# Kernel optimization log

Hardware: AMD Instinct MI355X
Metric: run time of the kernel (lower is better)

Reference implementation:

```python
import jax, jax.numpy as jnp
import numpy as np

D, B, L, LS, DH, DU, QK, CD = 5, 2048, 50, 50, 128, 128, 64, 64
EPS = 1e-5

def _l2norm(x):
    n = jnp.linalg.norm(x, axis=-1, keepdims=True)
    return x / jnp.maximum(n, 1e-12)

def setup_inputs() -> dict:
    key = jax.random.key(0)
    ks = jax.random.split(key, 20)
    def pw(k, shape):
        return jax.random.normal(k, shape, dtype=jnp.float32) * 0.02
    return {
        "u": jax.random.normal(ks[0], (B, DU), jnp.float32),
        "H_intra": jax.random.normal(ks[1], (D, B, L, DH), jnp.float32),
        "H_share": jax.random.normal(ks[2], (B, LS, DH), jnp.float32),
        "h": jax.random.normal(ks[3], (B, DH), jnp.float32),
        "domain_ids": jax.random.randint(ks[4], (B,), 0, D),
        "Wq": pw(ks[5], (DU + DH, QK)), "bq": jnp.zeros((QK,), jnp.float32),
        "Wki": pw(ks[6], (DH, QK)), "bki": jnp.zeros((QK,), jnp.float32),
        "Wvi": pw(ks[7], (DH, QK)), "bvi": jnp.zeros((QK,), jnp.float32),
        "Wks": pw(ks[8], (DH, QK)), "bks": jnp.zeros((QK,), jnp.float32),
        "Wvs": pw(ks[9], (DH, QK)), "bvs": jnp.zeros((QK,), jnp.float32),
        "Wf": pw(ks[10], (2 * QK, CD)), "bf": jnp.zeros((CD,), jnp.float32),
        "Wgb": pw(ks[11], (CD, 2 * DH)), "bgb": jnp.zeros((2 * DH,), jnp.float32),
    }

def reference(u, H_intra, H_share, h, domain_ids, Wq, bq, Wki, bki, Wvi, bvi,
              Wks, bks, Wvs, bvs, Wf, bf, Wgb, bgb):
    scale = jnp.sqrt(jnp.asarray(QK, jnp.float32))
    # ---- CDIExtractor (domain loop batched over leading D axis) ----
    c = H_intra.mean(axis=2)                                   # [D,B,DH] ctx = mean over L
    u_b = jnp.broadcast_to(u, (D, B, DU))
    Q = jnp.concatenate([u_b, c], axis=-1) @ Wq + bq            # [D,B,QK]
    Ki = H_intra @ Wki + bki                                    # [D,B,L,QK]
    Vi = H_intra @ Wvi + bvi
    Ks = H_share @ Wks + bks                                    # [B,LS,QK]
    Vs = H_share @ Wvs + bvs
    a_i = jax.nn.softmax(jnp.einsum('dbq,dblq->dbl', Q, Ki) / scale, axis=-1)
    h_i = jnp.einsum('dbl,dblq->dbq', a_i, Vi)                  # [D,B,QK]
    a_s = jax.nn.softmax(jnp.einsum('dbq,blq->dbl', Q, Ks) / scale, axis=-1)
    h_s = jnp.einsum('dbl,blq->dbq', a_s, Vs)                   # [D,B,QK]
    z = jnp.concatenate([h_i, h_s], axis=-1) @ Wf + bf          # [D,B,CD]
    # ---- contrastive loss (stacked as [B,D,QK] like torch.stack(dim=1)) ----
    hi = jnp.transpose(h_i, (1, 0, 2))
    hs = jnp.transpose(h_s, (1, 0, 2))
    ni, ns = _l2norm(hi), _l2norm(hs)
    pos_sim = jnp.sum(ni * ns, axis=-1)                         # [B,D]
    all_sim = jnp.einsum('bdq,beq->bde', ni, ni)                # [B,D,D]
    denom = jnp.exp(all_sim).sum(axis=-1)                       # [B,D]
    L_con = -jnp.mean(jnp.log(jnp.exp(pos_sim) / (denom + 1e-8) + 1e-8))
    # ---- CDIRInjector_Norm (domain-masked AdaNorm, segment statistics) ----
    onehot = jax.nn.one_hot(domain_ids, D, dtype=h.dtype)       # [B,D]
    cnt = jnp.maximum(onehot.sum(axis=0), 1.0)                  # [D]
    mean_d = (onehot.T @ h) / cnt[:, None]                      # [D,DH]
    var_d = (onehot.T @ (h * h)) / cnt[:, None] - mean_d ** 2   # biased var
    mu = mean_d[domain_ids]                                     # [B,DH]
    va = var_d[domain_ids]
    h_norm = (h - mu) / jnp.sqrt(va + EPS)
    z_sel = z[domain_ids, jnp.arange(B)]                        # [B,CD]
    gb = z_sel @ Wgb + bgb
    gamma, beta = jnp.split(gb, 2, axis=-1)
    out = gamma * h_norm + beta + h                             # [B,DH]
    return out, L_con
```

## Files before the change

### kernel.cpp

```cpp
#include <hip/hip_runtime.h>
#include <math.h>

#define D 5
#define B 2048
#define L 50
#define LS 50
#define DH 128
#define DU 128
#define QK 64
#define CD 64
#define EPS 1e-5f

__device__ __forceinline__ float wsum(float v) {
    v += __shfl_xor(v, 1, 64);
    v += __shfl_xor(v, 2, 64);
    v += __shfl_xor(v, 4, 64);
    v += __shfl_xor(v, 8, 64);
    v += __shfl_xor(v, 16, 64);
    v += __shfl_xor(v, 32, 64);
    return v;
}

__device__ __forceinline__ float wmax(float v) {
    v = fmaxf(v, __shfl_xor(v, 1, 64));
    v = fmaxf(v, __shfl_xor(v, 2, 64));
    v = fmaxf(v, __shfl_xor(v, 4, 64));
    v = fmaxf(v, __shfl_xor(v, 8, 64));
    v = fmaxf(v, __shfl_xor(v, 16, 64));
    v = fmaxf(v, __shfl_xor(v, 32, 64));
    return v;
}

__device__ __forceinline__ float gsum32(float v) {
    v += __shfl_xor(v, 1, 64);
    v += __shfl_xor(v, 2, 64);
    v += __shfl_xor(v, 4, 64);
    v += __shfl_xor(v, 8, 64);
    v += __shfl_xor(v, 16, 64);
    return v;
}

__device__ __forceinline__ float dot4(float4 a, float4 b) {
    return a.x * b.x + a.y * b.y + a.z * b.z + a.w * b.w;
}

__global__ __launch_bounds__(256) void ksetup(
    const float* __restrict__ u,
    const float* __restrict__ Wq, const float* __restrict__ bq,
    const float* __restrict__ Wki, const float* __restrict__ Wks,
    float* __restrict__ Gi, float* __restrict__ Gs,
    float* __restrict__ qu_i, float* __restrict__ qu_s)
{
    const int t = threadIdx.x;
    if (blockIdx.x < DH) {
        __shared__ float sWqc[QK];
        const int j = blockIdx.x;
        if (t < QK) sWqc[t] = Wq[(DU + j) * QK + t];
        __syncthreads();
        const int k = t & 127;
        const float* Wk = (t < 128) ? Wki : Wks;
        const float4* Wr = (const float4*)(Wk + k * QK);
        const float4* cq = (const float4*)sWqc;
        float acc = 0.f;
        #pragma unroll
        for (int q4 = 0; q4 < 16; ++q4) acc += dot4(Wr[q4], cq[q4]);
        if (t < 128) Gi[j * DH + k] = acc;
        else Gs[j * DH + k] = acc;
    } else {
        __shared__ float sPart[4 * QK];
        __shared__ float sQu[QK];
        const int b = blockIdx.x - DH;
        const int lane = t & 63, wave = t >> 6;
        float acc = 0.f;
        const int k0 = wave * 32;
        #pragma unroll 8
        for (int i = 0; i < 32; ++i) {
            int k = k0 + i;
            acc += u[(size_t)b * DU + k] * Wq[k * QK + lane];
        }
        sPart[wave * QK + lane] = acc;
        __syncthreads();
        if (t < QK) sQu[t] = bq[t] + sPart[t] + sPart[64 + t] + sPart[128 + t] + sPart[192 + t];
        __syncthreads();
        const int k = t & 127;
        const float* Wk = (t < 128) ? Wki : Wks;
        const float4* Wr = (const float4*)(Wk + k * QK);
        const float4* cq = (const float4*)sQu;
        float acc2 = 0.f;
        #pragma unroll
        for (int q4 = 0; q4 < 16; ++q4) acc2 += dot4(Wr[q4], cq[q4]);
        if (t < 128) qu_i[(size_t)b * DH + k] = acc2;
        else qu_s[(size_t)b * DH + k] = acc2;
    }
}

__global__ __launch_bounds__(256, 4) void kin(
    const float* __restrict__ Hi,
    const float* __restrict__ Gi, const float* __restrict__ Gs,
    const float* __restrict__ qu_i, const float* __restrict__ qu_s,
    const float* __restrict__ Wvi, const float* __restrict__ bvi,
    float* __restrict__ qvs_w,
    float* __restrict__ hi_w)
{
    __shared__ float4 sP4[256];
    __shared__ float sC2[2 * DH];
    __shared__ float sQVi[2 * DH];
    __shared__ float sSc[128];
    __shared__ float sA[128];
    __shared__ float sVagg[2 * DH];
    __shared__ float sPA[256], sPB[256];

    const int b0 = blockIdx.x * 2;
    const int d = blockIdx.y;
    const int t = threadIdx.x;
    const int lane = t & 63, wave = t >> 6;
    const int bb = t >> 7;
    const int tb = t & 127;
    const int gg = tb >> 5;
    const int col4 = t & 31;
    const int nr = (gg < 2) ? 13 : 12;
    const float* sPf = (const float*)sP4;

    const float* Hbase = Hi + ((size_t)d * B + (b0 + bb)) * (L * DH);
    float4 h4[13];
    #pragma unroll
    for (int k = 0; k < 13; ++k)
        if (k < nr) h4[k] = *(const float4*)(Hbase + (gg + 4 * k) * DH + 4 * col4);

    {
        float4 cs = make_float4(0.f, 0.f, 0.f, 0.f);
        #pragma unroll
        for (int k = 0; k < 13; ++k)
            if (k < nr) { cs.x += h4[k].x; cs.y += h4[k].y; cs.z += h4[k].z; cs.w += h4[k].w; }
        sP4[t] = cs;
    }
    __syncthreads();
    {
        const int bbc = t >> 7, col = t & 127;
        float s = sPf[bbc * 512 + col] + sPf[bbc * 512 + 128 + col]
                + sPf[bbc * 512 + 256 + col] + sPf[bbc * 512 + 384 + col];
        sC2[col * 2 + bbc] = s * (1.0f / (float)L);
    }
    __syncthreads();

    {
        const int mat = t >> 7, k = t & 127;
        const float* G = mat ? Gs : Gi;
        const float* qum = mat ? qu_s : qu_i;
        float a0 = qum[(size_t)b0 * DH + k];
        float a1 = qum[(size_t)(b0 + 1) * DH + k];
        const float2* c2 = (const float2*)sC2;
        #pragma unroll 8
        for (int j = 0; j < DH; ++j) {
            float g = G[j * DH + k];
            float2 c = c2[j];
            a0 += c.x * g;
            a1 += c.y * g;
        }
        if (mat == 0) { sQVi[k] = a0; sQVi[DH + k] = a1; }
        else {
            qvs_w[((size_t)d * B + b0) * DH + k] = a0;
            qvs_w[((size_t)d * B + b0 + 1) * DH + k] = a1;
        }
    }
    __syncthreads();

    {
        float4 qv = ((const float4*)sQVi)[bb * 32 + col4];
        #pragma unroll
        for (int k = 0; k < 13; ++k)
            if (k < nr) {
                float p = dot4(h4[k], qv);
                p = gsum32(p);
                if (col4 == 0) sSc[bb * 64 + gg + 4 * k] = p * 0.125f;
            }
    }
    __syncthreads();
    if (wave < 2) {
        float s = (lane < L) ? sSc[wave * 64 + lane] : -3.0e38f;
        float m = wmax(s);
        float e = (lane < L) ? expf(s - m) : 0.f;
        float ssum = wsum(e);
        if (lane < L) sA[wave * 64 + lane] = e / ssum;
    }
    __syncthreads();

    {
        float4 va = make_float4(0.f, 0.f, 0.f, 0.f);
        #pragma unroll
        for (int k = 0; k < 13; ++k)
            if (k < nr) {
                float a = sA[bb * 64 + gg + 4 * k];
                va.x += a * h4[k].x; va.y += a * h4[k].y;
                va.z += a * h4[k].z; va.w += a * h4[k].w;
            }
        sP4[t] = va;
    }
    __syncthreads();
    {
        const int bbc = t >> 7, col = t & 127;
        sVagg[bbc * 128 + col] = sPf[bbc * 512 + col] + sPf[bbc * 512 + 128 + col]
                               + sPf[bbc * 512 + 256 + col] + sPf[bbc * 512 + 384 + col];
    }
    __syncthreads();

    {
        const int q = t & 63, kq = t >> 6;
        const int k0 = kq * 32;
        float a0 = 0.f, a1 = 0.f;
        #pragma unroll 8
        for (int i = 0; i < 32; ++i) {
            int k = k0 + i;
            float w = Wvi[k * QK + q];
            a0 += sVagg[k] * w;
            a1 += sVagg[128 + k] * w;
        }
        sPA[kq * 64 + q] = a0;
        sPB[kq * 64 + q] = a1;
    }
    __syncthreads();
    if (t < 128) {
        const int bw = t >> 6, q = t & 63;
        const float* P = bw ? sPB : sPA;
        hi_w[((size_t)d * B + b0 + bw) * QK + q] =
            bvi[q] + P[q] + P[64 + q] + P[128 + q] + P[192 + q];
    }
}

__global__ __launch_bounds__(256) void kstat(
    const float* __restrict__ h, const int* __restrict__ dom_ids,
    float* __restrict__ gsum, float* __restrict__ gsq, float* __restrict__ gcnt)
{
    __shared__ float sS[D * DH], sQ2[D * DH], sCnt[D];
    const int t = threadIdx.x;
    const int b0 = blockIdx.x * 32;
    for (int i = t; i < D * DH; i += 256) { sS[i] = 0.f; sQ2[i] = 0.f; }
    if (t < D) sCnt[t] = 0.f;
    __syncthreads();
    const int col = t & 127, half = t >> 7;
    for (int rr = 0; rr < 16; ++rr) {
        int b = b0 + rr * 2 + half;
        float v = h[(size_t)b * DH + col];
        int dm = dom_ids[b];
        atomicAdd(&sS[dm * DH + col], v);
        atomicAdd(&sQ2[dm * DH + col], v * v);
        if (col == 0) atomicAdd(&sCnt[dm], 1.f);
    }
    __syncthreads();
    for (int i = t; i < D * DH; i += 256) {
        atomicAdd(&gsum[i], sS[i]);
        atomicAdd(&gsq[i], sQ2[i]);
    }
    if (t < D) atomicAdd(&gcnt[t], sCnt[t]);
}

__global__ __launch_bounds__(256, 4) void ksh(
    const float* __restrict__ Hs,
    const float* __restrict__ qvs_w,
    const float* __restrict__ Wvs, const float* __restrict__ bvs,
    float* __restrict__ hs_w)
{
    __shared__ float4 sQV4[160];
    __shared__ float sS[D * 64];
    __shared__ float4 sVP4[1280];
    __shared__ float sVA[D * DH];

    const int b = blockIdx.x;
    const int t = threadIdx.x;
    const int lane = t & 63;
    const int wave = t >> 6;
    const int g = t >> 5;
    const int col4 = t & 31;
    const int nrow = (g < 2) ? 7 : 6;
    float* sBigF = (float*)sVP4;

    const float* Hbase = Hs + (size_t)b * LS * DH;
    float4 h4[7];
    #pragma unroll
    for (int k = 0; k < 7; ++k)
        if (k < nrow) h4[k] = *(const float4*)(Hbase + (g + 8 * k) * DH + 4 * col4);
    if (t < 160) {
        int dd = t >> 5, c4 = t & 31;
        sQV4[t] = *(const float4*)(qvs_w + ((size_t)dd * B + b) * DH + 4 * c4);
    }
    __syncthreads();

    #pragma unroll
    for (int dd = 0; dd < D; ++dd) {
        float4 qv = sQV4[dd * 32 + col4];
        #pragma unroll
        for (int k = 0; k < 7; ++k)
            if (k < nrow) {
                float p = dot4(h4[k], qv);
                p = gsum32(p);
                if (col4 == 0) sS[dd * 64 + g + 8 * k] = p * 0.125f;
            }
    }
    __syncthreads();
    for (int dd = wave; dd < D; dd += 4) {
        float s = (lane < LS) ? sS[dd * 64 + lane] : -3.0e38f;
        float m = wmax(s);
        float e = (lane < LS) ? expf(s - m) : 0.f;
        float ssum = wsum(e);
        if (lane < LS) sS[dd * 64 + lane] = e / ssum;
    }
    __syncthreads();

    {
        float4 va[D];
        #pragma unroll
        for (int dd = 0; dd < D; ++dd) va[dd] = make_float4(0.f, 0.f, 0.f, 0.f);
        #pragma unroll
        for (int k = 0; k < 7; ++k)
            if (k < nrow) {
                float4 hv = h4[k];
                #pragma unroll
                for (int dd = 0; dd < D; ++dd) {
                    float a = sS[dd * 64 + g + 8 * k];
                    va[dd].x += a * hv.x; va[dd].y += a * hv.y;
                    va[dd].z += a * hv.z; va[dd].w += a * hv.w;
                }
            }
        #pragma unroll
        for (int dd = 0; dd < D; ++dd) sVP4[dd * 256 + t] = va[dd];
    }
    __syncthreads();
    for (int o = t; o < D * DH; o += 256) {
        int dd = o >> 7, col = o & 127;
        float s = 0.f;
        #pragma unroll
        for (int gg = 0; gg < 8; ++gg) s += sBigF[dd * 1024 + gg * 128 + col];
        sVA[o] = s;
    }
    __syncthreads();

    #pragma unroll
    for (int j = 0; j < 5; ++j) {
        int tau = t + j * 256;
        int kq = tau / 320;
        int o = tau - kq * 320;
        int dd = o >> 6, q = o & 63;
        float acc = 0.f;
        const int k0 = kq * 32;
        #pragma unroll 8
        for (int i = 0; i < 32; ++i) {
            int k = k0 + i;
            acc += sVA[dd * 128 + k] * Wvs[k * QK + q];
        }
        sBigF[tau] = acc;
    }
    __syncthreads();
    for (int o = t; o < D * QK; o += 256) {
        int dd = o >> 6, q = o & 63;
        hs_w[((size_t)dd * B + b) * QK + q] =
            bvs[q] + sBigF[o] + sBigF[o + 320] + sBigF[o + 640] + sBigF[o + 960];
    }
}

__global__ __launch_bounds__(256) void kfin(
    const float* __restrict__ h, const int* __restrict__ dom_ids,
    const float* __restrict__ hi_w, const float* __restrict__ hs_w,
    const float* __restrict__ Wf, const float* __restrict__ bf,
    const float* __restrict__ Wgb, const float* __restrict__ bgb,
    const float* __restrict__ gsum, const float* __restrict__ gsq,
    const float* __restrict__ gcnt,
    float* __restrict__ out, float* __restrict__ loss_out)
{
    __shared__ float sHI[D * QK], sHS[D * QK];
    __shared__ float sInv[16], sSim[32], sZ[QK], sPartZ[256], sGB[256];

    const int b = blockIdx.x;
    const int t = threadIdx.x;
    const int lane = t & 63;
    const int wave = t >> 6;
    const int dm = dom_ids[b];

    if (t < 80) {
        int dd = t >> 4, q4 = t & 15;
        ((float4*)sHI)[t] = *(const float4*)(hi_w + ((size_t)dd * B + b) * QK + 4 * q4);
        ((float4*)sHS)[t] = *(const float4*)(hs_w + ((size_t)dd * B + b) * QK + 4 * q4);
    }
    __syncthreads();

    for (int v = wave; v < 2 * D; v += 4) {
        float x = (v < D) ? sHI[v * QK + lane] : sHS[(v - D) * QK + lane];
        float ss = wsum(x * x);
        if (lane == 0) sInv[v] = 1.0f / fmaxf(sqrtf(ss), 1e-12f);
    }
    __syncthreads();
    for (int p = wave; p < 30; p += 4) {
        float s;
        if (p < 25) {
            int dd = p / 5, e = p - dd * 5;
            s = wsum(sHI[dd * QK + lane] * sHI[e * QK + lane] * sInv[dd] * sInv[e]);
        } else {
            int dd = p - 25;
            s = wsum(sHI[dd * QK + lane] * sHS[dd * QK + lane] * sInv[dd] * sInv[D + dd]);
        }
        if (lane == 0) sSim[p] = s;
    }
    __syncthreads();
    if (t == 0) {
        float tot = 0.f;
        #pragma unroll
        for (int dd = 0; dd < D; ++dd) {
            float den = 0.f;
            #pragma unroll
            for (int e = 0; e < D; ++e) den += expf(sSim[dd * 5 + e]);
            tot += logf(expf(sSim[25 + dd]) / (den + 1e-8f) + 1e-8f);
        }
        atomicAdd(loss_out, -tot / (float)(B * D));
    }

    {
        const int kq = wave, q = lane;
        float acc = 0.f;
        const int k0 = kq * 32;
        #pragma unroll 8
        for (int i = 0; i < 32; ++i) {
            int k = k0 + i;
            float x = (k < QK) ? sHI[dm * QK + k] : sHS[dm * QK + (k - QK)];
            acc += x * Wf[k * CD + q];
        }
        sPartZ[t] = acc;
    }
    __syncthreads();
    if (t < QK) sZ[t] = bf[t] + sPartZ[t] + sPartZ[64 + t] + sPartZ[128 + t] + sPartZ[192 + t];
    __syncthreads();

    {
        float acc = bgb[t];
        #pragma unroll 8
        for (int k = 0; k < CD; ++k) acc += sZ[k] * Wgb[k * (2 * DH) + t];
        sGB[t] = acc;
    }
    __syncthreads();

    if (t < DH) {
        float c = fmaxf(gcnt[dm], 1.0f);
        float mu = gsum[dm * DH + t] / c;
        float va = gsq[dm * DH + t] / c - mu * mu;
        float hv = h[(size_t)b * DH + t];
        float hn = (hv - mu) / sqrtf(va + EPS);
        out[(size_t)b * DH + t] = sGB[t] * hn + sGB[DH + t] + hv;
    }
}

extern "C" void kernel_launch(void* const* d_in, const int* in_sizes, int n_in,
                              void* d_out, int out_size, void* d_ws, size_t ws_size,
                              hipStream_t stream)
{
    (void)in_sizes; (void)n_in; (void)out_size; (void)ws_size;
    const float* u   = (const float*)d_in[0];
    const float* Hi  = (const float*)d_in[1];
    const float* Hs  = (const float*)d_in[2];
    const float* h   = (const float*)d_in[3];
    const int*   dom = (const int*)d_in[4];
    const float* Wq  = (const float*)d_in[5];
    const float* bq  = (const float*)d_in[6];
    const float* Wki = (const float*)d_in[7];
    const float* Wvi = (const float*)d_in[9];
    const float* bvi = (const float*)d_in[10];
    const float* Wks = (const float*)d_in[11];
    const float* Wvs = (const float*)d_in[13];
    const float* bvs = (const float*)d_in[14];
    const float* Wf  = (const float*)d_in[15];
    const float* bf  = (const float*)d_in[16];
    const float* Wgb = (const float*)d_in[17];
    const float* bgb = (const float*)d_in[18];

    float* out = (float*)d_out;
    float* loss_out = out + (size_t)B * DH;

    float* ws = (float*)d_ws;
    float* Gi    = ws;
    float* Gs    = Gi + DH * DH;
    float* qu_i  = Gs + DH * DH;
    float* qu_s  = qu_i + (size_t)B * DH;
    float* qvs_w = qu_s + (size_t)B * DH;
    float* hi_w  = qvs_w + (size_t)D * B * DH;
    float* hs_w  = hi_w + (size_t)D * B * QK;
    float* gsum  = hs_w + (size_t)D * B * QK;
    float* gsq   = gsum + D * DH;
    float* gcnt  = gsq + D * DH;

    hipMemsetAsync(gsum, 0, (size_t)(2 * D * DH + 8) * sizeof(float), stream);
    hipMemsetAsync(loss_out, 0, sizeof(float), stream);

    hipLaunchKernelGGL(ksetup, dim3(DH + B), dim3(256), 0, stream,
                       u, Wq, bq, Wki, Wks, Gi, Gs, qu_i, qu_s);
    hipLaunchKernelGGL(kstat, dim3(B / 32), dim3(256), 0, stream, h, dom, gsum, gsq, gcnt);
    hipLaunchKernelGGL(kin, dim3(B / 2, D), dim3(256), 0, stream,
                       Hi, Gi, Gs, qu_i, qu_s, Wvi, bvi, qvs_w, hi_w);
    hipLaunchKernelGGL(ksh, dim3(B), dim3(256), 0, stream, Hs, qvs_w, Wvs, bvs, hs_w);
    hipLaunchKernelGGL(kfin, dim3(B), dim3(256), 0, stream,
                       h, dom, hi_w, hs_w, Wf, bf, Wgb, bgb, gsum, gsq, gcnt, out, loss_out);
}
```

Measured before the change: 557.3 us.

## Transpose G and value weights for float4 row reads; shrink ksh reduction buffer

The setup kernel now writes the G matrices transposed and adds two blocks that transpose Wvi and Wvs. This lets the per-block matvecs in kin and ksh read contiguous float4 rows instead of strided scalars. ksh folds its value partials with a cross-half-wave shuffle before writing to shared memory, which halves the sVP4 buffer. Launch bounds rise to 5 blocks per SM for kin and ksh. The trade-off is two extra transpose blocks in setup, and per-thread row reads of GT that are no longer coalesced across threads.

```diff
diff --git a/kernel.cpp b/kernel.cpp
--- a/kernel.cpp
+++ b/kernel.cpp
@@ -48,12 +48,14 @@
     const float* __restrict__ u,
     const float* __restrict__ Wq, const float* __restrict__ bq,
     const float* __restrict__ Wki, const float* __restrict__ Wks,
-    float* __restrict__ Gi, float* __restrict__ Gs,
+    const float* __restrict__ Wvi, const float* __restrict__ Wvs,
+    float* __restrict__ GiT, float* __restrict__ GsT,
+    float* __restrict__ WviT, float* __restrict__ WvsT,
     float* __restrict__ qu_i, float* __restrict__ qu_s)
 {
     const int t = threadIdx.x;
     if (blockIdx.x < DH) {
-        __shared__ float sWqc[QK];
+        __shared__ __align__(16) float sWqc[QK];
         const int j = blockIdx.x;
         if (t < QK) sWqc[t] = Wq[(DU + j) * QK + t];
         __syncthreads();
@@ -64,12 +66,19 @@
         float acc = 0.f;
         #pragma unroll
         for (int q4 = 0; q4 < 16; ++q4) acc += dot4(Wr[q4], cq[q4]);
-        if (t < 128) Gi[j * DH + k] = acc;
-        else Gs[j * DH + k] = acc;
+        if (t < 128) GiT[k * DH + j] = acc;
+        else GsT[k * DH + j] = acc;
+    } else if (blockIdx.x < DH + 2) {
+        const float* W = (blockIdx.x == DH) ? Wvi : Wvs;
+        float* WT = (blockIdx.x == DH) ? WviT : WvsT;
+        for (int i = t; i < DH * QK; i += 256) {
+            int kk = i >> 6, q = i & 63;
+            WT[q * DH + kk] = W[i];
+        }
     } else {
         __shared__ float sPart[4 * QK];
-        __shared__ float sQu[QK];
-        const int b = blockIdx.x - DH;
+        __shared__ __align__(16) float sQu[QK];
+        const int b = blockIdx.x - DH - 2;
         const int lane = t & 63, wave = t >> 6;
         float acc = 0.f;
         const int k0 = wave * 32;
@@ -94,20 +103,21 @@
     }
 }
 
-__global__ __launch_bounds__(256, 4) void kin(
+__global__ __launch_bounds__(256, 5) void kin(
     const float* __restrict__ Hi,
-    const float* __restrict__ Gi, const float* __restrict__ Gs,
+    const float* __restrict__ GiT, const float* __restrict__ GsT,
     const float* __restrict__ qu_i, const float* __restrict__ qu_s,
-    const float* __restrict__ Wvi, const float* __restrict__ bvi,
+    const float* __restrict__ WviT, const float* __restrict__ bvi,
     float* __restrict__ qvs_w,
     float* __restrict__ hi_w)
 {
     __shared__ float4 sP4[256];
-    __shared__ float sC2[2 * DH];
-    __shared__ float sQVi[2 * DH];
+    __shared__ __align__(16) float sC0[DH];
+    __shared__ __align__(16) float sC1[DH];
+    __shared__ __align__(16) float sQVi[2 * DH];
     __shared__ float sSc[128];
     __shared__ float sA[128];
-    __shared__ float sVagg[2 * DH];
+    __shared__ __align__(16) float sVagg[2 * DH];
     __shared__ float sPA[256], sPB[256];
 
     const int b0 = blockIdx.x * 2;
@@ -139,23 +149,25 @@
         const int bbc = t >> 7, col = t & 127;
         float s = sPf[bbc * 512 + col] + sPf[bbc * 512 + 128 + col]
                 + sPf[bbc * 512 + 256 + col] + sPf[bbc * 512 + 384 + col];
-        sC2[col * 2 + bbc] = s * (1.0f / (float)L);
+        float* sc = bbc ? sC1 : sC0;
+        sc[col] = s * (1.0f / (float)L);
     }
     __syncthreads();
 
     {
         const int mat = t >> 7, k = t & 127;
-        const float* G = mat ? Gs : Gi;
+        const float* GT = mat ? GsT : GiT;
         const float* qum = mat ? qu_s : qu_i;
         float a0 = qum[(size_t)b0 * DH + k];
         float a1 = qum[(size_t)(b0 + 1) * DH + k];
-        const float2* c2 = (const float2*)sC2;
+        const float4* Gr = (const float4*)(GT + (size_t)k * DH);
+        const float4* c0 = (const float4*)sC0;
+        const float4* c1 = (const float4*)sC1;
         #pragma unroll 8
-        for (int j = 0; j < DH; ++j) {
-            float g = G[j * DH + k];
-            float2 c = c2[j];
-            a0 += c.x * g;
-            a1 += c.y * g;
+        for (int j4 = 0; j4 < 32; ++j4) {
+            float4 g = Gr[j4];
+            a0 += dot4(g, c0[j4]);
+            a1 += dot4(g, c1[j4]);
         }
         if (mat == 0) { sQVi[k] = a0; sQVi[DH + k] = a1; }
         else {
@@ -206,14 +218,15 @@
 
     {
         const int q = t & 63, kq = t >> 6;
-        const int k0 = kq * 32;
+        const float4* Wr = (const float4*)(WviT + q * DH + kq * 32);
+        const float4* v0 = (const float4*)(sVagg + kq * 32);
+        const float4* v1 = (const float4*)(sVagg + DH + kq * 32);
         float a0 = 0.f, a1 = 0.f;
-        #pragma unroll 8
-        for (int i = 0; i < 32; ++i) {
-            int k = k0 + i;
-            float w = Wvi[k * QK + q];
-            a0 += sVagg[k] * w;
-            a1 += sVagg[128 + k] * w;
+        #pragma unroll
+        for (int i = 0; i < 8; ++i) {
+            float4 w = Wr[i];
+            a0 += dot4(w, v0[i]);
+            a1 += dot4(w, v1[i]);
         }
         sPA[kq * 64 + q] = a0;
         sPB[kq * 64 + q] = a1;
@@ -254,16 +267,16 @@
     if (t < D) atomicAdd(&gcnt[t], sCnt[t]);
 }
 
-__global__ __launch_bounds__(256, 4) void ksh(
+__global__ __launch_bounds__(256, 5) void ksh(
     const float* __restrict__ Hs,
     const float* __restrict__ qvs_w,
-    const float* __restrict__ Wvs, const float* __restrict__ bvs,
+    const float* __restrict__ WvsT, const float* __restrict__ bvs,
     float* __restrict__ hs_w)
 {
     __shared__ float4 sQV4[160];
     __shared__ float sS[D * 64];
-    __shared__ float4 sVP4[1280];
-    __shared__ float sVA[D * DH];
+    __shared__ float4 sVP4[640];
+    __shared__ __align__(16) float sVA[D * DH];
 
     const int b = blockIdx.x;
     const int t = threadIdx.x;
@@ -322,14 +335,24 @@
                 }
             }
         #pragma unroll
-        for (int dd = 0; dd < D; ++dd) sVP4[dd * 256 + t] = va[dd];
+        for (int dd = 0; dd < D; ++dd) {
+            va[dd].x += __shfl_xor(va[dd].x, 32, 64);
+            va[dd].y += __shfl_xor(va[dd].y, 32, 64);
+            va[dd].z += __shfl_xor(va[dd].z, 32, 64);
+            va[dd].w += __shfl_xor(va[dd].w, 32, 64);
+        }
+        if (lane < 32) {
+            #pragma unroll
+            for (int dd = 0; dd < D; ++dd)
+                sVP4[(dd * 4 + wave) * 32 + col4] = va[dd];
+        }
     }
     __syncthreads();
     for (int o = t; o < D * DH; o += 256) {
         int dd = o >> 7, col = o & 127;
         float s = 0.f;
         #pragma unroll
-        for (int gg = 0; gg < 8; ++gg) s += sBigF[dd * 1024 + gg * 128 + col];
+        for (int gh = 0; gh < 4; ++gh) s += sBigF[(dd * 4 + gh) * 128 + col];
         sVA[o] = s;
     }
     __syncthreads();
@@ -340,13 +363,11 @@
         int kq = tau / 320;
         int o = tau - kq * 320;
         int dd = o >> 6, q = o & 63;
+        const float4* Wr = (const float4*)(WvsT + q * DH + kq * 32);
+        const float4* vv = (const float4*)(sVA + dd * DH + kq * 32);
         float acc = 0.f;
-        const int k0 = kq * 32;
-        #pragma unroll 8
-        for (int i = 0; i < 32; ++i) {
-            int k = k0 + i;
-            acc += sVA[dd * 128 + k] * Wvs[k * QK + q];
-        }
+        #pragma unroll
+        for (int i = 0; i < 8; ++i) acc += dot4(Wr[i], vv[i]);
         sBigF[tau] = acc;
     }
     __syncthreads();
@@ -366,7 +387,8 @@
     const float* __restrict__ gcnt,
     float* __restrict__ out, float* __restrict__ loss_out)
 {
-    __shared__ float sHI[D * QK], sHS[D * QK];
+    __shared__ __align__(16) float sHI[D * QK];
+    __shared__ __align__(16) float sHS[D * QK];
     __shared__ float sInv[16], sSim[32], sZ[QK], sPartZ[256], sGB[256];
 
     const int b = blockIdx.x;
@@ -473,9 +495,11 @@
     float* loss_out = out + (size_t)B * DH;
 
     float* ws = (float*)d_ws;
-    float* Gi    = ws;
-    float* Gs    = Gi + DH * DH;
-    float* qu_i  = Gs + DH * DH;
+    float* GiT   = ws;
+    float* GsT   = GiT + DH * DH;
+    float* WviT  = GsT + DH * DH;
+    float* WvsT  = WviT + QK * DH;
+    float* qu_i  = WvsT + QK * DH;
     float* qu_s  = qu_i + (size_t)B * DH;
     float* qvs_w = qu_s + (size_t)B * DH;
     float* hi_w  = qvs_w + (size_t)D * B * DH;
@@ -487,12 +511,12 @@
     hipMemsetAsync(gsum, 0, (size_t)(2 * D * DH + 8) * sizeof(float), stream);
     hipMemsetAsync(loss_out, 0, sizeof(float), stream);
 
-    hipLaunchKernelGGL(ksetup, dim3(DH + B), dim3(256), 0, stream,
-                       u, Wq, bq, Wki, Wks, Gi, Gs, qu_i, qu_s);
+    hipLaunchKernelGGL(ksetup, dim3(DH + 2 + B), dim3(256), 0, stream,
+                       u, Wq, bq, Wki, Wks, Wvi, Wvs, GiT, GsT, WviT, WvsT, qu_i, qu_s);
     hipLaunchKernelGGL(kstat, dim3(B / 32), dim3(256), 0, stream, h, dom, gsum, gsq, gcnt);
     hipLaunchKernelGGL(kin, dim3(B / 2, D), dim3(256), 0, stream,
-                       Hi, Gi, Gs, qu_i, qu_s, Wvi, bvi, qvs_w, hi_w);
-    hipLaunchKernelGGL(ksh, dim3(B), dim3(256), 0, stream, Hs, qvs_w, Wvs, bvs, hs_w);
+                       Hi, GiT, GsT, qu_i, qu_s, WviT, bvi, qvs_w, hi_w);
+    hipLaunchKernelGGL(ksh, dim3(B), dim3(256), 0, stream, Hs, qvs_w, WvsT, bvs, hs_w);
     hipLaunchKernelGGL(kfin, dim3(B), dim3(256), 0, stream,
                        h, dom, hi_w, hs_w, Wf, bf, Wgb, bgb, gsum, gsq, gcnt, out, loss_out);
 }
```

After: 627.0 us. 12.5% more time.
